# Optimization experiments

Hardware: AMD Instinct MI355X
Metric: run time of the kernel (lower is better)

## Reference

```python
import jax, jax.numpy as jnp
import numpy as np

N, CIN, H, W = 32, 1024, 32, 32
C, CT, L = 1024, 1024, 16
HEAD, GROUPS = 16, 16
GS = C // GROUPS  # 64, group size == head dim


def setup_inputs() -> dict:
    key = jax.random.key(0)
    ks = jax.random.split(key, 8)
    s = 0.02
    return {
        "feature": jax.random.normal(ks[0], (N, CIN, H, W), jnp.float32),
        "token": jax.random.normal(ks[1], (N, CT, L), jnp.float32),
        # conv_query: Conv1d(CT, C, k=1) -> dense [C, CT] + bias [C]
        "Wq": jax.random.normal(ks[2], (C, CT), jnp.float32) * s,
        "bq": jax.random.normal(ks[3], (C,), jnp.float32) * s,
        # conv_key / conv_value: grouped Conv2d(C, C, k=1, groups=16) -> block-diag [G, GS, GS]
        "Wk": jax.random.normal(ks[4], (GROUPS, GS, GS), jnp.float32) * s,
        "bk": jax.random.normal(ks[5], (C,), jnp.float32) * s,
        "Wv": jax.random.normal(ks[6], (GROUPS, GS, GS), jnp.float32) * s,
        "bv": jax.random.normal(ks[7], (C,), jnp.float32) * s,
    }


def reference(feature, token, Wq, bq, Wk, bk, Wv, bv):
    n, c, h, w = feature.shape  # c == C (feature-proj branch skipped)
    hw = h * w
    hd = C // HEAD  # 64
    l = token.shape[2]

    # conv_query (1x1 conv1d == dense over channels): [N, C, L]
    query = jnp.einsum('oc,ncl->nol', Wq, token) + bq[None, :, None]
    query = query.reshape(n, HEAD, hd, l)  # [N, head, hd, L]

    # grouped 1x1 convs == per-group 64x64 matmul over spatial positions
    f = feature.reshape(n, GROUPS, GS, hw)  # [N, G, GS, HW]
    key_ = jnp.einsum('goi,ngix->ngox', Wk, f) + bk.reshape(1, GROUPS, GS, 1)
    key_ = key_.reshape(n, HEAD, hd, hw)  # groups == head, same channel layout
    value = jnp.einsum('goi,ngix->ngox', Wv, f) + bv.reshape(1, GROUPS, GS, 1)
    value = value.reshape(n, HEAD, hd, hw)

    # cross attention: coef[n,h,x,l] = <key[:,x], query[:,l]> / sqrt(hd)
    coef = jnp.einsum('nhdx,nhdl->nhxl', key_, query) / jnp.sqrt(jnp.asarray(hd, jnp.float32))
    coef = jax.nn.softmax(coef, axis=2)  # softmax over spatial dim HW

    tok = jnp.einsum('nhdx,nhxl->nhdl', value, coef)  # [N, head, hd, L]
    # torch: .view(N, C, -1).view(N, L, C) — raw memory reshape, NOT transpose
    tok = tok.reshape(n, C, l).reshape(n, l, C)
    return (feature, tok)
```

## Files before the change

kernel.cpp:

```cpp
#include <hip/hip_runtime.h>
#include <math.h>

#define NB    32
#define NHEAD 16
#define HW    1024

typedef float f32x4  __attribute__((ext_vector_type(4)));
typedef short bf16x2 __attribute__((ext_vector_type(2)));
typedef short bf16x4 __attribute__((ext_vector_type(4)));
typedef short bf16x8 __attribute__((ext_vector_type(8)));

__device__ __forceinline__ short f2bf(float f) {
    union { float f; unsigned u; } c; c.f = f;
    unsigned r = c.u + 0x7FFFu + ((c.u >> 16) & 1u);
    return (short)(r >> 16);
}
#define SWZ(row) ((((row) >> 1) & 7) << 4)
#define MFMA16(a, b, c) __builtin_amdgcn_mfma_f32_16x16x32_bf16(a, b, c, 0, 0, 0)

__device__ __forceinline__ bf16x8 lds_ld8(const short* base, int off) {
    return *(const bf16x8*)((const char*)base + off);
}
__device__ __forceinline__ void lds_st4(short* base, int off, bf16x4 v) {
    *(bf16x4*)((char*)base + off) = v;
}

__global__ __launch_bounds__(256) void prep_kernel(
        const float* __restrict__ Wq, const float* __restrict__ token,
        const float* __restrict__ Wk, const float* __restrict__ bq,
        short* __restrict__ Wq_bf, short* __restrict__ tok_t,
        short* __restrict__ Wk_t, float* __restrict__ qkb) {
    __shared__ float red[256];
    const int b = blockIdx.x, t = threadIdx.x;
    if (b < 1024) {
        const size_t idx = (size_t)b * 1024 + t * 4;
        const f32x4 v = *(const f32x4*)(Wq + idx);
        bf16x4 o; o[0]=f2bf(v[0]); o[1]=f2bf(v[1]); o[2]=f2bf(v[2]); o[3]=f2bf(v[3]);
        *(bf16x4*)(Wq_bf + idx) = o;
    } else if (b < 1056) {
        const int n = b - 1024;
        const int c0 = t * 4;
        float arr[4][16];
#pragma unroll
        for (int ci = 0; ci < 4; ++ci)
#pragma unroll
            for (int lq = 0; lq < 4; ++lq) {
                const f32x4 v = *(const f32x4*)(token + (size_t)n*16384 + (size_t)(c0+ci)*16 + lq*4);
#pragma unroll
                for (int e = 0; e < 4; ++e) arr[ci][lq*4+e] = v[e];
            }
#pragma unroll
        for (int l = 0; l < 16; ++l) {
            bf16x4 o; o[0]=f2bf(arr[0][l]); o[1]=f2bf(arr[1][l]); o[2]=f2bf(arr[2][l]); o[3]=f2bf(arr[3][l]);
            *(bf16x4*)(tok_t + (size_t)n*16384 + (size_t)l*1024 + c0) = o;
        }
    } else {
        const int h = b - 1056;
        const int i = t & 63, dq = t >> 6;
        float qs = 0.f; short wt[16];
#pragma unroll
        for (int k = 0; k < 16; ++k) {
            const int d = dq*16 + k;
            const float wv = Wk[(size_t)h*4096 + d*64 + i];
            qs += wv * bq[h*64 + d];
            wt[k] = f2bf(wv);
        }
#pragma unroll
        for (int kq = 0; kq < 4; ++kq) {
            bf16x4 o; o[0]=wt[kq*4]; o[1]=wt[kq*4+1]; o[2]=wt[kq*4+2]; o[3]=wt[kq*4+3];
            *(bf16x4*)(Wk_t + (size_t)h*4096 + i*64 + dq*16 + kq*4) = o;
        }
        red[t] = qs;
        __syncthreads();
        if (t < 64)
            qkb[h*64 + t] = (red[t] + red[t+64] + red[t+128] + red[t+192]) * 0.125f;
    }
}

__global__ __launch_bounds__(256) void queryqk_kernel(
        const short* __restrict__ Wq_bf, const short* __restrict__ tok_t,
        const short* __restrict__ Wk_t, const float* __restrict__ qkb,
        short* __restrict__ qk_bf) {
    __shared__ short q_ld[16 * 64];
    const int t = threadIdx.x, w = t >> 6, L = t & 63;
    const int lr = L & 15, hg = L >> 4;
    const int nh = blockIdx.x, n = nh >> 4, h = nh & 15;

    f32x4 acc = {0.f, 0.f, 0.f, 0.f};
    const short* aA = Wq_bf + (size_t)(h*64 + w*16 + lr) * 1024 + hg*8;
    const short* aB = tok_t + (size_t)n*16384 + (size_t)lr*1024 + hg*8;
#pragma unroll 4
    for (int ks = 0; ks < 32; ++ks) {
        const bf16x8 a = *(const bf16x8*)(aA + ks*32);
        const bf16x8 bb = *(const bf16x8*)(aB + ks*32);
        acc = MFMA16(a, bb, acc);
    }
    {
        bf16x4 qv; qv[0]=f2bf(acc[0]); qv[1]=f2bf(acc[1]); qv[2]=f2bf(acc[2]); qv[3]=f2bf(acc[3]);
        lds_st4(q_ld, (lr*128 + w*32 + hg*8) ^ SWZ(lr), qv);
    }
    __syncthreads();
    f32x4 a2 = {0.f, 0.f, 0.f, 0.f};
#pragma unroll
    for (int ks = 0; ks < 2; ++ks) {
        const bf16x8 a = *(const bf16x8*)(Wk_t + (size_t)h*4096 + (w*16 + lr)*64 + ks*32 + hg*8);
        const bf16x8 bb = lds_ld8(q_ld, (lr*128 + ks*64 + hg*16) ^ SWZ(lr));
        a2 = MFMA16(a, bb, a2);
    }
    const int i0 = w*16 + hg*4;
    bf16x4 qk4;
#pragma unroll
    for (int r = 0; r < 4; ++r)
        qk4[r] = f2bf(a2[r] * 0.125f + qkb[h*64 + i0 + r]);
    *(bf16x4*)(qk_bf + (size_t)nh*1024 + lr*64 + i0) = qk4;
}

__global__ __launch_bounds__(1024, 4) void attn_kernel(
        const float* __restrict__ feat, const short* __restrict__ qk_bf,
        const float* __restrict__ Wv, const float* __restrict__ bv,
        float* __restrict__ out0, float* __restrict__ out1) {
    __shared__ __align__(16) short f_xi[32 * 1024];
    __shared__ __align__(16) short f_ix[32 * 1024];
    __shared__ __align__(16) short wv_ld[64 * 64];
    __shared__ __align__(16) short fcn_ld[16 * 64];
    __shared__ float red_m[256], red_z[256];

    const int t = threadIdx.x, w = t >> 6, L = t & 63;
    const int lr = L & 15, hg = L >> 4;
    const int nh = blockIdx.x, n = nh >> 4, h = nh & 15;
    const size_t fbase = (size_t)n*1048576 + (size_t)h*65536;

    const bf16x8 qb0 = *(const bf16x8*)(qk_bf + (size_t)nh*1024 + lr*64 + hg*8);
    const bf16x8 qb1 = *(const bf16x8*)(qk_bf + (size_t)nh*1024 + lr*64 + 32 + hg*8);
    const f32x4 wv4 = *(const f32x4*)(Wv + (size_t)h*4096 + (t>>4)*64 + (t&15)*4);

    f32x4 v[8];
    {
        const size_t rb = fbase + (size_t)(w*2) * 1024;
#pragma unroll
        for (int xr = 0; xr < 4; ++xr) {
            v[2*xr]   = *(const f32x4*)(feat + rb + xr*256 + L*4);
            v[2*xr+1] = *(const f32x4*)(feat + rb + 1024 + xr*256 + L*4);
        }
    }

    f32x4 S[4];
#pragma unroll
    for (int tl = 0; tl < 4; ++tl) S[tl] = (f32x4){0.f, 0.f, 0.f, 0.f};
    bf16x8 fcA[4][2];

#pragma unroll
    for (int c = 0; c < 2; ++c) {
        {
            const size_t rb = fbase + (size_t)(c*32 + w*2) * 1024;
            const int il0 = w*2, il1 = w*2 + 1;
#pragma unroll
            for (int xr = 0; xr < 4; ++xr) {
                const int x0 = xr*256 + L*4;
                const f32x4 v0 = v[2*xr], v1 = v[2*xr+1];
                *(f32x4*)(out0 + rb + x0) = v0;
                *(f32x4*)(out0 + rb + 1024 + x0) = v1;
                bf16x4 b0; b0[0]=f2bf(v0[0]); b0[1]=f2bf(v0[1]); b0[2]=f2bf(v0[2]); b0[3]=f2bf(v0[3]);
                bf16x4 b1; b1[0]=f2bf(v1[0]); b1[1]=f2bf(v1[1]); b1[2]=f2bf(v1[2]); b1[3]=f2bf(v1[3]);
                lds_st4(f_ix, il0*2048 + ((x0*2) ^ ((il0&7)<<4)), b0);
                lds_st4(f_ix, il1*2048 + ((x0*2) ^ ((il1&7)<<4)), b1);
#pragma unroll
                for (int j = 0; j < 4; ++j) {
                    const int x = x0 + j;
                    bf16x2 pr; pr[0] = f2bf(v0[j]); pr[1] = f2bf(v1[j]);
                    const int off = ((x>>1)<<7) + ((((x&1)<<6) + w*4) ^ (((x>>2)&7)<<4));
                    *(bf16x2*)((char*)f_xi + off) = pr;
                }
            }
            if (c == 0) {
                const size_t rb1 = fbase + (size_t)(32 + w*2) * 1024;
#pragma unroll
                for (int xr = 0; xr < 4; ++xr) {
                    v[2*xr]   = *(const f32x4*)(feat + rb1 + xr*256 + L*4);
                    v[2*xr+1] = *(const f32x4*)(feat + rb1 + 1024 + xr*256 + L*4);
                }
            }
        }
        __syncthreads();
        {
            const bf16x8 qb = c ? qb1 : qb0;
#pragma unroll
            for (int tl = 0; tl < 4; ++tl) {
                const int x = w*64 + tl*16 + lr;
                const int off = ((x>>1)<<7) + ((((x&1)<<6) + (hg<<4)) ^ (((x>>2)&7)<<4));
                S[tl] = MFMA16(*(const bf16x8*)((const char*)f_xi + off), qb, S[tl]);
            }
#pragma unroll
            for (int tl2 = 0; tl2 < 2; ++tl2) {
                const int il_m = tl2*16 + lr;
                const int base = il_m*2048, swz = (il_m&7)<<4;
                fcA[c*2 + tl2][0] = lds_ld8(f_ix, base + ((w*128      + hg*16) ^ swz));
                fcA[c*2 + tl2][1] = lds_ld8(f_ix, base + ((w*128 + 64 + hg*16) ^ swz));
            }
        }
        __syncthreads();
    }

    float m_l = -INFINITY;
#pragma unroll
    for (int tl = 0; tl < 4; ++tl)
#pragma unroll
        for (int r = 0; r < 4; ++r) m_l = fmaxf(m_l, S[tl][r]);
    m_l = fmaxf(m_l, __shfl_xor(m_l, 16));
    m_l = fmaxf(m_l, __shfl_xor(m_l, 32));
    if (L < 16) red_m[w*16 + L] = m_l;
    __syncthreads();
    float m_g = -INFINITY;
#pragma unroll
    for (int k = 0; k < 16; ++k) m_g = fmaxf(m_g, red_m[k*16 + lr]);
    float zl = 0.f;
#pragma unroll
    for (int tl = 0; tl < 4; ++tl)
#pragma unroll
        for (int r = 0; r < 4; ++r) {
            S[tl][r] = __expf(S[tl][r] - m_g);
            zl += S[tl][r];
        }
#pragma unroll
    for (int tl = 0; tl < 4; ++tl) {
        bf16x4 pv; pv[0]=f2bf(S[tl][0]); pv[1]=f2bf(S[tl][1]); pv[2]=f2bf(S[tl][2]); pv[3]=f2bf(S[tl][3]);
        *(bf16x4*)((char*)f_xi + w*2048 + lr*128 + ((tl*32 + hg*8) ^ ((lr&7)<<4))) = pv;
    }
    zl += __shfl_xor(zl, 16);
    zl += __shfl_xor(zl, 32);
    if (L < 16) red_z[w*16 + L] = zl;
    {
        const int d = t >> 4, i4 = (t & 15) * 4;
        bf16x4 wb; wb[0]=f2bf(wv4[0]); wb[1]=f2bf(wv4[1]); wb[2]=f2bf(wv4[2]); wb[3]=f2bf(wv4[3]);
        *(bf16x4*)((char*)wv_ld + d*128 + ((i4*2) ^ ((d&7)<<4))) = wb;
    }
    __syncthreads();
    float Zg = 0.f;
#pragma unroll
    for (int k = 0; k < 16; ++k) Zg += red_z[k*16 + lr];
    const float rz = 1.f / Zg;
    const bf16x8 pb0 = *(const bf16x8*)((const char*)f_xi + w*2048 + lr*128 + ((     hg*16) ^ ((lr&7)<<4)));
    const bf16x8 pb1 = *(const bf16x8*)((const char*)f_xi + w*2048 + lr*128 + ((64 + hg*16) ^ ((lr&7)<<4)));

#pragma unroll
    for (int ct = 0; ct < 4; ++ct) {
        f32x4 acc = (f32x4){0.f, 0.f, 0.f, 0.f};
        acc = MFMA16(fcA[ct][0], pb0, acc);
        acc = MFMA16(fcA[ct][1], pb1, acc);
        *(f32x4*)((char*)f_ix + w*4096 + ct*1024 + L*16) = acc;
    }
    __syncthreads();

    if (w < 4) {
        f32x4 sum = (f32x4){0.f, 0.f, 0.f, 0.f};
#pragma unroll
        for (int wp = 0; wp < 16; ++wp)
            sum += *(const f32x4*)((const char*)f_ix + wp*4096 + w*1024 + L*16);
        bf16x4 fb;
#pragma unroll
        for (int r = 0; r < 4; ++r) fb[r] = f2bf(sum[r] * rz);
        *(bf16x4*)((char*)fcn_ld + lr*128 + ((w*32 + hg*8) ^ ((lr&7)<<4))) = fb;
    }
    __syncthreads();
    if (w < 4) {
        f32x4 acc = (f32x4){0.f, 0.f, 0.f, 0.f};
        const int d_m = w*16 + lr;
#pragma unroll
        for (int ks = 0; ks < 2; ++ks) {
            const bf16x8 a = lds_ld8(wv_ld, d_m*128 + ((ks*64 + hg*16) ^ ((d_m&7)<<4)));
            const bf16x8 b = lds_ld8(fcn_ld, lr*128 + ((ks*64 + hg*16) ^ ((lr&7)<<4)));
            acc = MFMA16(a, b, acc);
        }
#pragma unroll
        for (int r = 0; r < 4; ++r) {
            const int d = w*16 + hg*4 + r;
            out1[((size_t)n*1024 + h*64 + d)*16 + lr] = acc[r] + bv[h*64 + d];
        }
    }
}

extern "C" void kernel_launch(void* const* d_in, const int* in_sizes, int n_in,
                              void* d_out, int out_size, void* d_ws, size_t ws_size,
                              hipStream_t stream) {
    const float* feature = (const float*)d_in[0];
    const float* token   = (const float*)d_in[1];
    const float* Wq      = (const float*)d_in[2];
    const float* bq      = (const float*)d_in[3];
    const float* Wk      = (const float*)d_in[4];
    const float* Wv      = (const float*)d_in[6];
    const float* bv      = (const float*)d_in[7];

    float* out0 = (float*)d_out;
    float* out1 = out0 + (size_t)NB * 1024 * HW;

    short* Wq_bf = (short*)d_ws;
    short* tok_t = Wq_bf + (size_t)1024 * 1024;
    short* Wk_t  = tok_t + (size_t)NB * 16 * 1024;
    short* qk_bf = Wk_t + (size_t)NHEAD * 64 * 64;
    float* qkb   = (float*)(qk_bf + (size_t)NB * NHEAD * 1024);

    prep_kernel   <<<dim3(1072), 256, 0, stream>>>(Wq, token, Wk, bq, Wq_bf, tok_t, Wk_t, qkb);
    queryqk_kernel<<<dim3(NB * NHEAD), 256, 0, stream>>>(Wq_bf, tok_t, Wk_t, qkb, qk_bf);
    attn_kernel   <<<dim3(NB * NHEAD), 1024, 0, stream>>>(feature, qk_bf, Wv, bv, out0, out1);
}
```

Before: 75.73 us.

## Make each wave own a private LDS region and re-read features for PV

Each wave now loads only the 64-column spatial slice it owns and transposes it into a private 4 KB LDS region, so the QK phase no longer needs the two block-wide barriers per channel chunk. The second LDS copy of the features is gone. The P·F stage instead re-reads the features from global memory and converts them to bf16 in registers. This shrinks LDS use from about 128 KB to 32 KB plus small buffers, which allows more blocks per CU and fewer barriers, at the cost of reading the feature tile from global memory twice (likely served from cache).

Result: slower. 90.16 us (+19.1%).

```diff
diff --git a/kernel.cpp b/kernel.cpp
--- a/kernel.cpp
+++ b/kernel.cpp
@@ -15,7 +15,8 @@
     unsigned r = c.u + 0x7FFFu + ((c.u >> 16) & 1u);
     return (short)(r >> 16);
 }
-#define SWZ(row) ((((row) >> 1) & 7) << 4)
+#define SWZ(row)  ((((row) >> 1) & 7) << 4)
+#define SW64(x)   ((((x) >> 1) & 3) << 4)
 #define MFMA16(a, b, c) __builtin_amdgcn_mfma_f32_16x16x32_bf16(a, b, c, 0, 0, 0)
 
 __device__ __forceinline__ bf16x8 lds_ld8(const short* base, int off) {
@@ -119,8 +120,7 @@
         const float* __restrict__ feat, const short* __restrict__ qk_bf,
         const float* __restrict__ Wv, const float* __restrict__ bv,
         float* __restrict__ out0, float* __restrict__ out1) {
-    __shared__ __align__(16) short f_xi[32 * 1024];
-    __shared__ __align__(16) short f_ix[32 * 1024];
+    __shared__ __align__(16) short f_lds[16 * 2048];
     __shared__ __align__(16) short wv_ld[64 * 64];
     __shared__ __align__(16) short fcn_ld[16 * 64];
     __shared__ float red_m[256], red_z[256];
@@ -129,76 +129,51 @@
     const int lr = L & 15, hg = L >> 4;
     const int nh = blockIdx.x, n = nh >> 4, h = nh & 15;
     const size_t fbase = (size_t)n*1048576 + (size_t)h*65536;
+    char* region = (char*)f_lds + w*4096;
 
     const bf16x8 qb0 = *(const bf16x8*)(qk_bf + (size_t)nh*1024 + lr*64 + hg*8);
     const bf16x8 qb1 = *(const bf16x8*)(qk_bf + (size_t)nh*1024 + lr*64 + 32 + hg*8);
-    const f32x4 wv4 = *(const f32x4*)(Wv + (size_t)h*4096 + (t>>4)*64 + (t&15)*4);
-
-    f32x4 v[8];
-    {
-        const size_t rb = fbase + (size_t)(w*2) * 1024;
-#pragma unroll
-        for (int xr = 0; xr < 4; ++xr) {
-            v[2*xr]   = *(const f32x4*)(feat + rb + xr*256 + L*4);
-            v[2*xr+1] = *(const f32x4*)(feat + rb + 1024 + xr*256 + L*4);
-        }
-    }
+
+    const int xseg = (L & 15) * 4;
+    const int ip   = (L >> 4) * 2;
+    const size_t xoff = (size_t)w*64 + xseg;
 
     f32x4 S[4];
 #pragma unroll
     for (int tl = 0; tl < 4; ++tl) S[tl] = (f32x4){0.f, 0.f, 0.f, 0.f};
-    bf16x8 fcA[4][2];
 
 #pragma unroll
     for (int c = 0; c < 2; ++c) {
-        {
-            const size_t rb = fbase + (size_t)(c*32 + w*2) * 1024;
-            const int il0 = w*2, il1 = w*2 + 1;
-#pragma unroll
-            for (int xr = 0; xr < 4; ++xr) {
-                const int x0 = xr*256 + L*4;
-                const f32x4 v0 = v[2*xr], v1 = v[2*xr+1];
-                *(f32x4*)(out0 + rb + x0) = v0;
-                *(f32x4*)(out0 + rb + 1024 + x0) = v1;
-                bf16x4 b0; b0[0]=f2bf(v0[0]); b0[1]=f2bf(v0[1]); b0[2]=f2bf(v0[2]); b0[3]=f2bf(v0[3]);
-                bf16x4 b1; b1[0]=f2bf(v1[0]); b1[1]=f2bf(v1[1]); b1[2]=f2bf(v1[2]); b1[3]=f2bf(v1[3]);
-                lds_st4(f_ix, il0*2048 + ((x0*2) ^ ((il0&7)<<4)), b0);
-                lds_st4(f_ix, il1*2048 + ((x0*2) ^ ((il1&7)<<4)), b1);
-#pragma unroll
-                for (int j = 0; j < 4; ++j) {
-                    const int x = x0 + j;
-                    bf16x2 pr; pr[0] = f2bf(v0[j]); pr[1] = f2bf(v1[j]);
-                    const int off = ((x>>1)<<7) + ((((x&1)<<6) + w*4) ^ (((x>>2)&7)<<4));
-                    *(bf16x2*)((char*)f_xi + off) = pr;
-                }
+        f32x4 v[8];
+#pragma unroll
+        for (int tk = 0; tk < 4; ++tk) {
+            const size_t r0 = fbase + (size_t)(c*32 + tk*8 + ip)*1024 + xoff;
+            v[2*tk]   = *(const f32x4*)(feat + r0);
+            v[2*tk+1] = *(const f32x4*)(feat + r0 + 1024);
+        }
+#pragma unroll
+        for (int tk = 0; tk < 4; ++tk) {
+            const size_t r0 = fbase + (size_t)(c*32 + tk*8 + ip)*1024 + xoff;
+            *(f32x4*)(out0 + r0)        = v[2*tk];
+            *(f32x4*)(out0 + r0 + 1024) = v[2*tk+1];
+        }
+#pragma unroll
+        for (int tk = 0; tk < 4; ++tk) {
+            const int il = tk*8 + ip;
+#pragma unroll
+            for (int j = 0; j < 4; ++j) {
+                const int x = xseg + j;
+                bf16x2 pr; pr[0] = f2bf(v[2*tk][j]); pr[1] = f2bf(v[2*tk+1][j]);
+                *(bf16x2*)(region + x*64 + ((il*2) ^ SW64(x))) = pr;
             }
-            if (c == 0) {
-                const size_t rb1 = fbase + (size_t)(32 + w*2) * 1024;
-#pragma unroll
-                for (int xr = 0; xr < 4; ++xr) {
-                    v[2*xr]   = *(const f32x4*)(feat + rb1 + xr*256 + L*4);
-                    v[2*xr+1] = *(const f32x4*)(feat + rb1 + 1024 + xr*256 + L*4);
-                }
-            }
-        }
-        __syncthreads();
-        {
-            const bf16x8 qb = c ? qb1 : qb0;
-#pragma unroll
-            for (int tl = 0; tl < 4; ++tl) {
-                const int x = w*64 + tl*16 + lr;
-                const int off = ((x>>1)<<7) + ((((x&1)<<6) + (hg<<4)) ^ (((x>>2)&7)<<4));
-                S[tl] = MFMA16(*(const bf16x8*)((const char*)f_xi + off), qb, S[tl]);
-            }
-#pragma unroll
-            for (int tl2 = 0; tl2 < 2; ++tl2) {
-                const int il_m = tl2*16 + lr;
-                const int base = il_m*2048, swz = (il_m&7)<<4;
-                fcA[c*2 + tl2][0] = lds_ld8(f_ix, base + ((w*128      + hg*16) ^ swz));
-                fcA[c*2 + tl2][1] = lds_ld8(f_ix, base + ((w*128 + 64 + hg*16) ^ swz));
-            }
-        }
-        __syncthreads();
+        }
+        const bf16x8 qb = c ? qb1 : qb0;
+#pragma unroll
+        for (int tl = 0; tl < 4; ++tl) {
+            const int x = tl*16 + lr;
+            const bf16x8 a = *(const bf16x8*)(region + x*64 + ((hg*16) ^ SW64(x)));
+            S[tl] = MFMA16(a, qb, S[tl]);
+        }
     }
 
     float m_l = -INFINITY;
@@ -224,13 +199,14 @@
 #pragma unroll
     for (int tl = 0; tl < 4; ++tl) {
         bf16x4 pv; pv[0]=f2bf(S[tl][0]); pv[1]=f2bf(S[tl][1]); pv[2]=f2bf(S[tl][2]); pv[3]=f2bf(S[tl][3]);
-        *(bf16x4*)((char*)f_xi + w*2048 + lr*128 + ((tl*32 + hg*8) ^ ((lr&7)<<4))) = pv;
+        *(bf16x4*)(region + lr*128 + ((tl*32 + hg*8) ^ ((lr&7)<<4))) = pv;
     }
     zl += __shfl_xor(zl, 16);
     zl += __shfl_xor(zl, 32);
     if (L < 16) red_z[w*16 + L] = zl;
     {
         const int d = t >> 4, i4 = (t & 15) * 4;
+        const f32x4 wv4 = *(const f32x4*)(Wv + (size_t)h*4096 + d*64 + i4);
         bf16x4 wb; wb[0]=f2bf(wv4[0]); wb[1]=f2bf(wv4[1]); wb[2]=f2bf(wv4[2]); wb[3]=f2bf(wv4[3]);
         *(bf16x4*)((char*)wv_ld + d*128 + ((i4*2) ^ ((d&7)<<4))) = wb;
     }
@@ -239,15 +215,26 @@
 #pragma unroll
     for (int k = 0; k < 16; ++k) Zg += red_z[k*16 + lr];
     const float rz = 1.f / Zg;
-    const bf16x8 pb0 = *(const bf16x8*)((const char*)f_xi + w*2048 + lr*128 + ((     hg*16) ^ ((lr&7)<<4)));
-    const bf16x8 pb1 = *(const bf16x8*)((const char*)f_xi + w*2048 + lr*128 + ((64 + hg*16) ^ ((lr&7)<<4)));
+    const bf16x8 pb0 = *(const bf16x8*)(region + lr*128 + ((     hg*16) ^ ((lr&7)<<4)));
+    const bf16x8 pb1 = *(const bf16x8*)(region + lr*128 + ((64 + hg*16) ^ ((lr&7)<<4)));
 
 #pragma unroll
     for (int ct = 0; ct < 4; ++ct) {
+        const size_t ro = fbase + (size_t)(ct*16 + lr)*1024 + w*64;
+        const f32x4 g0 = *(const f32x4*)(feat + ro + hg*8);
+        const f32x4 g1 = *(const f32x4*)(feat + ro + hg*8 + 4);
+        const f32x4 g2 = *(const f32x4*)(feat + ro + 32 + hg*8);
+        const f32x4 g3 = *(const f32x4*)(feat + ro + 32 + hg*8 + 4);
+        bf16x8 A0, A1;
+#pragma unroll
+        for (int e = 0; e < 4; ++e) {
+            A0[e] = f2bf(g0[e]); A0[4+e] = f2bf(g1[e]);
+            A1[e] = f2bf(g2[e]); A1[4+e] = f2bf(g3[e]);
+        }
         f32x4 acc = (f32x4){0.f, 0.f, 0.f, 0.f};
-        acc = MFMA16(fcA[ct][0], pb0, acc);
-        acc = MFMA16(fcA[ct][1], pb1, acc);
-        *(f32x4*)((char*)f_ix + w*4096 + ct*1024 + L*16) = acc;
+        acc = MFMA16(A0, pb0, acc);
+        acc = MFMA16(A1, pb1, acc);
+        *(f32x4*)(region + ct*1024 + L*16) = acc;
     }
     __syncthreads();
 
@@ -255,7 +242,7 @@
         f32x4 sum = (f32x4){0.f, 0.f, 0.f, 0.f};
 #pragma unroll
         for (int wp = 0; wp < 16; ++wp)
-            sum += *(const f32x4*)((const char*)f_ix + wp*4096 + w*1024 + L*16);
+            sum += *(const f32x4*)((const char*)f_lds + wp*4096 + w*1024 + L*16);
         bf16x4 fb;
 #pragma unroll
         for (int r = 0; r < 4; ++r) fb[r] = f2bf(sum[r] * rz);
```

## Restructure attention kernel into streaming online-softmax over spatial chunks with 512 threads

Applied to the files above, without the earlier changes.

The attention kernel now uses 512 threads and processes the 1024 spatial positions in four chunks of 256. Each chunk runs an online (flash-style) softmax with running max and sum, and folds P·F into register accumulators as it goes, instead of staging all of feature in LDS and doing a global softmax first. This cuts LDS footprint and barriers and overlaps prefetching the next chunk with compute. In exchange it adds rescaling work and more shuffle reductions per chunk.

New measurement: 135.1 us. +78.4%, slower.

```diff
diff --git a/kernel.cpp b/kernel.cpp
--- a/kernel.cpp
+++ b/kernel.cpp
@@ -16,6 +16,9 @@
     return (short)(r >> 16);
 }
 #define SWZ(row) ((((row) >> 1) & 7) << 4)
+#define SWX(x)   ((((x) >> 2) & 7) << 4)
+#define SWI(i)   ((((i) & 7)) << 4)
+#define SWL(l)   ((((l) & 7)) << 4)
 #define MFMA16(a, b, c) __builtin_amdgcn_mfma_f32_16x16x32_bf16(a, b, c, 0, 0, 0)
 
 __device__ __forceinline__ bf16x8 lds_ld8(const short* base, int off) {
@@ -115,160 +118,172 @@
     *(bf16x4*)(qk_bf + (size_t)nh*1024 + lr*64 + i0) = qk4;
 }
 
-__global__ __launch_bounds__(1024, 4) void attn_kernel(
+__global__ __launch_bounds__(512, 4) void attn_kernel(
         const float* __restrict__ feat, const short* __restrict__ qk_bf,
         const float* __restrict__ Wv, const float* __restrict__ bv,
         float* __restrict__ out0, float* __restrict__ out1) {
-    __shared__ __align__(16) short f_xi[32 * 1024];
-    __shared__ __align__(16) short f_ix[32 * 1024];
-    __shared__ __align__(16) short wv_ld[64 * 64];
-    __shared__ __align__(16) short fcn_ld[16 * 64];
-    __shared__ float red_m[256], red_z[256];
+    __shared__ __align__(16) short fx[256 * 64];
+    __shared__ __align__(16) short fi[64 * 256];
+    __shared__ __align__(16) short p_scr[8 * 640];
+    __shared__ __align__(16) short fcn[16 * 64];
+    __shared__ float red_m[128], red_z[128];
 
     const int t = threadIdx.x, w = t >> 6, L = t & 63;
     const int lr = L & 15, hg = L >> 4;
     const int nh = blockIdx.x, n = nh >> 4, h = nh & 15;
     const size_t fbase = (size_t)n*1048576 + (size_t)h*65536;
 
-    const bf16x8 qb0 = *(const bf16x8*)(qk_bf + (size_t)nh*1024 + lr*64 + hg*8);
-    const bf16x8 qb1 = *(const bf16x8*)(qk_bf + (size_t)nh*1024 + lr*64 + 32 + hg*8);
-    const f32x4 wv4 = *(const f32x4*)(Wv + (size_t)h*4096 + (t>>4)*64 + (t&15)*4);
+    const bf16x8 qkA0 = *(const bf16x8*)(qk_bf + (size_t)nh*1024 + lr*64 + hg*8);
+    const bf16x8 qkA1 = *(const bf16x8*)(qk_bf + (size_t)nh*1024 + lr*64 + 32 + hg*8);
+
+    const int sx = (t & 63) * 4;
+    const int si = (t >> 6) * 8;
+    short* p_w = p_scr + w * 640;
 
     f32x4 v[8];
+#pragma unroll
+    for (int k = 0; k < 8; ++k)
+        v[k] = *(const f32x4*)(feat + fbase + (size_t)(si+k)*1024 + sx);
+
+    f32x4 acc_fc[4];
+#pragma unroll
+    for (int ct = 0; ct < 4; ++ct) acc_fc[ct] = (f32x4){0.f,0.f,0.f,0.f};
+    float mrun[4] = {-INFINITY,-INFINITY,-INFINITY,-INFINITY};
+    float Zrun[4] = {0.f,0.f,0.f,0.f};
+
+#pragma unroll
+    for (int c = 0; c < 4; ++c) {
+        bf16x4 vb[8];
+#pragma unroll
+        for (int k = 0; k < 8; ++k) {
+            vb[k][0]=f2bf(v[k][0]); vb[k][1]=f2bf(v[k][1]);
+            vb[k][2]=f2bf(v[k][2]); vb[k][3]=f2bf(v[k][3]);
+        }
+#pragma unroll
+        for (int k = 0; k < 8; ++k) {
+            const size_t g = fbase + (size_t)(si+k)*1024 + c*256 + sx;
+            *(f32x4*)(out0 + g) = v[k];
+            lds_st4(fi, ((si+k)*512 + sx*2) ^ SWI(si+k), vb[k]);
+        }
+#pragma unroll
+        for (int j = 0; j < 4; ++j) {
+            const int x = sx + j;
+#pragma unroll
+            for (int kp = 0; kp < 4; ++kp) {
+                const int i2 = si + 2*kp;
+                bf16x2 pr; pr[0] = vb[2*kp][j]; pr[1] = vb[2*kp+1][j];
+                *(bf16x2*)((char*)fx + ((x*128 + i2*2) ^ SWX(x))) = pr;
+            }
+        }
+        __syncthreads();
+        if (c < 3) {
+#pragma unroll
+            for (int k = 0; k < 8; ++k)
+                v[k] = *(const f32x4*)(feat + fbase + (size_t)(si+k)*1024 + (c+1)*256 + sx);
+        }
+        f32x4 ST0 = {0.f,0.f,0.f,0.f}, ST1 = {0.f,0.f,0.f,0.f};
+        {
+            const int xb0 = w*32 + lr, xb1 = w*32 + 16 + lr;
+            ST0 = MFMA16(qkA0, lds_ld8(fx, (xb0*128 + hg*16)      ^ SWX(xb0)), ST0);
+            ST0 = MFMA16(qkA1, lds_ld8(fx, (xb0*128 + 64 + hg*16) ^ SWX(xb0)), ST0);
+            ST1 = MFMA16(qkA0, lds_ld8(fx, (xb1*128 + hg*16)      ^ SWX(xb1)), ST1);
+            ST1 = MFMA16(qkA1, lds_ld8(fx, (xb1*128 + 64 + hg*16) ^ SWX(xb1)), ST1);
+        }
+#pragma unroll
+        for (int r = 0; r < 4; ++r) {
+            float cm = fmaxf(ST0[r], ST1[r]);
+#pragma unroll
+            for (int msk = 8; msk >= 1; msk >>= 1)
+                cm = fmaxf(cm, __shfl_xor(cm, msk));
+            const float mnew = fmaxf(mrun[r], cm);
+            const float rs = __expf(mrun[r] - mnew);
+            const float p0 = __expf(ST0[r] - mnew);
+            const float p1 = __expf(ST1[r] - mnew);
+            const int row = (hg*4 + r) * 80;
+            *(short*)((char*)p_w + row + lr*2)      = f2bf(p0);
+            *(short*)((char*)p_w + row + 32 + lr*2) = f2bf(p1);
+            float zc = p0 + p1;
+#pragma unroll
+            for (int msk = 8; msk >= 1; msk >>= 1)
+                zc += __shfl_xor(zc, msk);
+            Zrun[r] = Zrun[r] * rs + zc;
+            mrun[r] = mnew;
+#pragma unroll
+            for (int ct = 0; ct < 4; ++ct) acc_fc[ct][r] *= rs;
+        }
+        {
+            const bf16x8 pA = lds_ld8(p_w, lr*80 + hg*16);
+#pragma unroll
+            for (int ct = 0; ct < 4; ++ct) {
+                const int i = ct*16 + lr;
+                const bf16x8 fB = lds_ld8(fi, (i*512 + w*64 + hg*16) ^ SWI(i));
+                acc_fc[ct] = MFMA16(pA, fB, acc_fc[ct]);
+            }
+        }
+        __syncthreads();
+    }
+
+    if (lr == 0) {
+#pragma unroll
+        for (int r = 0; r < 4; ++r) {
+            red_m[w*16 + hg*4 + r] = mrun[r];
+            red_z[w*16 + hg*4 + r] = Zrun[r];
+        }
+    }
+    __syncthreads();
     {
-        const size_t rb = fbase + (size_t)(w*2) * 1024;
-#pragma unroll
-        for (int xr = 0; xr < 4; ++xr) {
-            v[2*xr]   = *(const f32x4*)(feat + rb + xr*256 + L*4);
-            v[2*xr+1] = *(const f32x4*)(feat + rb + 1024 + xr*256 + L*4);
-        }
-    }
-
-    f32x4 S[4];
-#pragma unroll
-    for (int tl = 0; tl < 4; ++tl) S[tl] = (f32x4){0.f, 0.f, 0.f, 0.f};
-    bf16x8 fcA[4][2];
-
-#pragma unroll
-    for (int c = 0; c < 2; ++c) {
-        {
-            const size_t rb = fbase + (size_t)(c*32 + w*2) * 1024;
-            const int il0 = w*2, il1 = w*2 + 1;
-#pragma unroll
-            for (int xr = 0; xr < 4; ++xr) {
-                const int x0 = xr*256 + L*4;
-                const f32x4 v0 = v[2*xr], v1 = v[2*xr+1];
-                *(f32x4*)(out0 + rb + x0) = v0;
-                *(f32x4*)(out0 + rb + 1024 + x0) = v1;
-                bf16x4 b0; b0[0]=f2bf(v0[0]); b0[1]=f2bf(v0[1]); b0[2]=f2bf(v0[2]); b0[3]=f2bf(v0[3]);
-                bf16x4 b1; b1[0]=f2bf(v1[0]); b1[1]=f2bf(v1[1]); b1[2]=f2bf(v1[2]); b1[3]=f2bf(v1[3]);
-                lds_st4(f_ix, il0*2048 + ((x0*2) ^ ((il0&7)<<4)), b0);
-                lds_st4(f_ix, il1*2048 + ((x0*2) ^ ((il1&7)<<4)), b1);
-#pragma unroll
-                for (int j = 0; j < 4; ++j) {
-                    const int x = x0 + j;
-                    bf16x2 pr; pr[0] = f2bf(v0[j]); pr[1] = f2bf(v1[j]);
-                    const int off = ((x>>1)<<7) + ((((x&1)<<6) + w*4) ^ (((x>>2)&7)<<4));
-                    *(bf16x2*)((char*)f_xi + off) = pr;
-                }
-            }
-            if (c == 0) {
-                const size_t rb1 = fbase + (size_t)(32 + w*2) * 1024;
-#pragma unroll
-                for (int xr = 0; xr < 4; ++xr) {
-                    v[2*xr]   = *(const f32x4*)(feat + rb1 + xr*256 + L*4);
-                    v[2*xr+1] = *(const f32x4*)(feat + rb1 + 1024 + xr*256 + L*4);
-                }
-            }
-        }
-        __syncthreads();
-        {
-            const bf16x8 qb = c ? qb1 : qb0;
-#pragma unroll
-            for (int tl = 0; tl < 4; ++tl) {
-                const int x = w*64 + tl*16 + lr;
-                const int off = ((x>>1)<<7) + ((((x&1)<<6) + (hg<<4)) ^ (((x>>2)&7)<<4));
-                S[tl] = MFMA16(*(const bf16x8*)((const char*)f_xi + off), qb, S[tl]);
-            }
-#pragma unroll
-            for (int tl2 = 0; tl2 < 2; ++tl2) {
-                const int il_m = tl2*16 + lr;
-                const int base = il_m*2048, swz = (il_m&7)<<4;
-                fcA[c*2 + tl2][0] = lds_ld8(f_ix, base + ((w*128      + hg*16) ^ swz));
-                fcA[c*2 + tl2][1] = lds_ld8(f_ix, base + ((w*128 + 64 + hg*16) ^ swz));
-            }
-        }
-        __syncthreads();
-    }
-
-    float m_l = -INFINITY;
-#pragma unroll
-    for (int tl = 0; tl < 4; ++tl)
-#pragma unroll
-        for (int r = 0; r < 4; ++r) m_l = fmaxf(m_l, S[tl][r]);
-    m_l = fmaxf(m_l, __shfl_xor(m_l, 16));
-    m_l = fmaxf(m_l, __shfl_xor(m_l, 32));
-    if (L < 16) red_m[w*16 + L] = m_l;
-    __syncthreads();
-    float m_g = -INFINITY;
-#pragma unroll
-    for (int k = 0; k < 16; ++k) m_g = fmaxf(m_g, red_m[k*16 + lr]);
-    float zl = 0.f;
-#pragma unroll
-    for (int tl = 0; tl < 4; ++tl)
-#pragma unroll
-        for (int r = 0; r < 4; ++r) {
-            S[tl][r] = __expf(S[tl][r] - m_g);
-            zl += S[tl][r];
-        }
-#pragma unroll
-    for (int tl = 0; tl < 4; ++tl) {
-        bf16x4 pv; pv[0]=f2bf(S[tl][0]); pv[1]=f2bf(S[tl][1]); pv[2]=f2bf(S[tl][2]); pv[3]=f2bf(S[tl][3]);
-        *(bf16x4*)((char*)f_xi + w*2048 + lr*128 + ((tl*32 + hg*8) ^ ((lr&7)<<4))) = pv;
-    }
-    zl += __shfl_xor(zl, 16);
-    zl += __shfl_xor(zl, 32);
-    if (L < 16) red_z[w*16 + L] = zl;
+        const int d = t >> 3, i0 = (t & 7) * 8;
+        const f32x4 a = *(const f32x4*)(Wv + (size_t)h*4096 + d*64 + i0);
+        const f32x4 b = *(const f32x4*)(Wv + (size_t)h*4096 + d*64 + i0 + 4);
+        bf16x8 wb;
+        wb[0]=f2bf(a[0]); wb[1]=f2bf(a[1]); wb[2]=f2bf(a[2]); wb[3]=f2bf(a[3]);
+        wb[4]=f2bf(b[0]); wb[5]=f2bf(b[1]); wb[6]=f2bf(b[2]); wb[7]=f2bf(b[3]);
+        *(bf16x8*)((char*)fi + ((d*128 + i0*2) ^ SWL(d))) = wb;
+    }
     {
-        const int d = t >> 4, i4 = (t & 15) * 4;
-        bf16x4 wb; wb[0]=f2bf(wv4[0]); wb[1]=f2bf(wv4[1]); wb[2]=f2bf(wv4[2]); wb[3]=f2bf(wv4[3]);
-        *(bf16x4*)((char*)wv_ld + d*128 + ((i4*2) ^ ((d&7)<<4))) = wb;
-    }
-    __syncthreads();
-    float Zg = 0.f;
-#pragma unroll
-    for (int k = 0; k < 16; ++k) Zg += red_z[k*16 + lr];
-    const float rz = 1.f / Zg;
-    const bf16x8 pb0 = *(const bf16x8*)((const char*)f_xi + w*2048 + lr*128 + ((     hg*16) ^ ((lr&7)<<4)));
-    const bf16x8 pb1 = *(const bf16x8*)((const char*)f_xi + w*2048 + lr*128 + ((64 + hg*16) ^ ((lr&7)<<4)));
-
-#pragma unroll
-    for (int ct = 0; ct < 4; ++ct) {
-        f32x4 acc = (f32x4){0.f, 0.f, 0.f, 0.f};
-        acc = MFMA16(fcA[ct][0], pb0, acc);
-        acc = MFMA16(fcA[ct][1], pb1, acc);
-        *(f32x4*)((char*)f_ix + w*4096 + ct*1024 + L*16) = acc;
-    }
-    __syncthreads();
-
-    if (w < 4) {
-        f32x4 sum = (f32x4){0.f, 0.f, 0.f, 0.f};
-#pragma unroll
-        for (int wp = 0; wp < 16; ++wp)
-            sum += *(const f32x4*)((const char*)f_ix + wp*4096 + w*1024 + L*16);
-        bf16x4 fb;
-#pragma unroll
-        for (int r = 0; r < 4; ++r) fb[r] = f2bf(sum[r] * rz);
-        *(bf16x4*)((char*)fcn_ld + lr*128 + ((w*32 + hg*8) ^ ((lr&7)<<4))) = fb;
+        float sc[4];
+#pragma unroll
+        for (int r = 0; r < 4; ++r) {
+            const int l = hg*4 + r;
+            float m = red_m[l];
+#pragma unroll
+            for (int wp = 1; wp < 8; ++wp) m = fmaxf(m, red_m[wp*16 + l]);
+            sc[r] = __expf(mrun[r] - m);
+        }
+#pragma unroll
+        for (int ct = 0; ct < 4; ++ct) {
+#pragma unroll
+            for (int r = 0; r < 4; ++r) acc_fc[ct][r] *= sc[r];
+            *(f32x4*)((char*)fx + (w*4 + ct)*1024 + L*16) = acc_fc[ct];
+        }
     }
     __syncthreads();
     if (w < 4) {
-        f32x4 acc = (f32x4){0.f, 0.f, 0.f, 0.f};
-        const int d_m = w*16 + lr;
+        f32x4 s = (f32x4){0.f,0.f,0.f,0.f};
+#pragma unroll
+        for (int wp = 0; wp < 8; ++wp)
+            s += *(const f32x4*)((const char*)fx + (wp*4 + w)*1024 + L*16);
+#pragma unroll
+        for (int r = 0; r < 4; ++r) {
+            const int l = hg*4 + r;
+            float m = red_m[l];
+#pragma unroll
+            for (int wp = 1; wp < 8; ++wp) m = fmaxf(m, red_m[wp*16 + l]);
+            float Z = 0.f;
+#pragma unroll
+            for (int wp = 0; wp < 8; ++wp)
+                Z += __expf(red_m[wp*16 + l] - m) * red_z[wp*16 + l];
+            *(short*)((char*)fcn + ((l*128 + (w*16 + lr)*2) ^ SWL(l))) = f2bf(s[r] / Z);
+        }
+    }
+    __syncthreads();
+    if (w < 4) {
+        f32x4 acc = (f32x4){0.f,0.f,0.f,0.f};
+        const int dm = w*16 + lr;
 #pragma unroll
         for (int ks = 0; ks < 2; ++ks) {
-            const bf16x8 a = lds_ld8(wv_ld, d_m*128 + ((ks*64 + hg*16) ^ ((d_m&7)<<4)));
-            const bf16x8 b = lds_ld8(fcn_ld, lr*128 + ((ks*64 + hg*16) ^ ((lr&7)<<4)));
+            const bf16x8 a = lds_ld8(fi,  (dm*128 + ks*64 + hg*16) ^ SWL(dm));
+            const bf16x8 b = lds_ld8(fcn, (lr*128 + ks*64 + hg*16) ^ SWL(lr));
             acc = MFMA16(a, b, acc);
         }
 #pragma unroll
@@ -301,5 +316,5 @@
 
     prep_kernel   <<<dim3(1072), 256, 0, stream>>>(Wq, token, Wk, bq, Wq_bf, tok_t, Wk_t, qkb);
     queryqk_kernel<<<dim3(NB * NHEAD), 256, 0, stream>>>(Wq_bf, tok_t, Wk_t, qkb, qk_bf);
-    attn_kernel   <<<dim3(NB * NHEAD), 1024, 0, stream>>>(feature, qk_bf, Wv, bv, out0, out1);
-}
+    attn_kernel   <<<dim3(NB * NHEAD), 512, 0, stream>>>(feature, qk_bf, Wv, bv, out0, out1);
+}
```
